# Kernel tuning notes

Measured on AMD Instinct MI355X. Metric: run time of the kernel, lower is better.

Reference implementation:

```python
import jax, jax.numpy as jnp
import numpy as np

N_C, N_A = 300000, 100000        # customers, articles
D_IN, H = 128, 128               # input feature dim, hidden dim
E, E_LBL = 2000000, 1000000      # message edges, supervision edges
BN_EPS = 1e-5


def setup_inputs() -> dict:
    key = jax.random.key(0)
    ks = jax.random.split(key, 18)
    w = lambda k, shape: jax.random.normal(k, shape, jnp.float32) * 0.05
    return {
        # node features
        "x_customer": jax.random.normal(ks[0], (N_C, D_IN), jnp.float32),
        "x_article": jax.random.normal(ks[1], (N_A, D_IN), jnp.float32),
        # customer->article edges (reverse direction reuses the same pairs)
        "edge_src_customer": jax.random.randint(ks[2], (E,), 0, N_C),
        "edge_dst_article": jax.random.randint(ks[3], (E,), 0, N_A),
        # supervision (label) edges for the decoder
        "label_customer": jax.random.randint(ks[4], (E_LBL,), 0, N_C),
        "label_article": jax.random.randint(ks[5], (E_LBL,), 0, N_A),
        # encoder layer 1 (per edge type: msg weight + self weight + bias)
        "W_msg1_ca": w(ks[6], (D_IN, H)), "W_self1_a": w(ks[7], (D_IN, H)), "b1_a": jnp.zeros((H,), jnp.float32),
        "W_msg1_ac": w(ks[8], (D_IN, H)), "W_self1_c": w(ks[9], (D_IN, H)), "b1_c": jnp.zeros((H,), jnp.float32),
        # encoder layer 2
        "W_msg2_ca": w(ks[10], (H, H)), "W_self2_a": w(ks[11], (H, H)), "b2_a": jnp.zeros((H,), jnp.float32),
        "W_msg2_ac": w(ks[12], (H, H)), "W_self2_c": w(ks[13], (H, H)), "b2_c": jnp.zeros((H,), jnp.float32),
        # per-node-type batch norm params
        "bn_gamma_c": jnp.ones((H,), jnp.float32), "bn_beta_c": jnp.zeros((H,), jnp.float32),
        "bn_gamma_a": jnp.ones((H,), jnp.float32), "bn_beta_a": jnp.zeros((H,), jnp.float32),
        # decoder MLP: Linear(2H->H) + relu, Linear(H->1)
        "W_dec1": w(ks[14], (2 * H, H)), "b_dec1": jnp.zeros((H,), jnp.float32),
        "W_dec2": w(ks[15], (H, 1)), "b_dec2": jnp.zeros((1,), jnp.float32),
    }


def _sage(x_src, x_dst, src, dst, n_dst, W_msg, W_self, b):
    # SAGEConv-style: mean-aggregate src features over incoming edges, then linear.
    agg = jax.ops.segment_sum(x_src[src], dst, num_segments=n_dst)          # [n_dst, d]
    cnt = jax.ops.segment_sum(jnp.ones((src.shape[0], 1), x_src.dtype), dst,
                              num_segments=n_dst)                            # [n_dst, 1]
    mean = agg / jnp.maximum(cnt, 1.0)
    return mean @ W_msg + x_dst @ W_self + b


def _bn(x, gamma, beta):
    # training-mode batch norm over the node axis, per channel
    mu = x.mean(axis=0)
    var = x.var(axis=0)
    return gamma * (x - mu) * jax.lax.rsqrt(var + BN_EPS) + beta


def reference(x_customer, x_article, edge_src_customer, edge_dst_article,
              label_customer, label_article,
              W_msg1_ca, W_self1_a, b1_a, W_msg1_ac, W_self1_c, b1_c,
              W_msg2_ca, W_self2_a, b2_a, W_msg2_ac, W_self2_c, b2_c,
              bn_gamma_c, bn_beta_c, bn_gamma_a, bn_beta_a,
              W_dec1, b_dec1, W_dec2, b_dec2):
    src_c, dst_a = edge_src_customer, edge_dst_article
    # hetero encoder, layer 1 (relu on all but the last layer)
    h_a = jax.nn.relu(_sage(x_customer, x_article, src_c, dst_a, N_A,
                            W_msg1_ca, W_self1_a, b1_a))
    h_c = jax.nn.relu(_sage(x_article, x_customer, dst_a, src_c, N_C,
                            W_msg1_ac, W_self1_c, b1_c))
    # layer 2 (no activation)
    z_a = _sage(h_c, h_a, src_c, dst_a, N_A, W_msg2_ca, W_self2_a, b2_a)
    z_c = _sage(h_a, h_c, dst_a, src_c, N_C, W_msg2_ac, W_self2_c, b2_c)
    # per-node-type batch norm
    z_c = _bn(z_c, bn_gamma_c, bn_beta_c)
    z_a = _bn(z_a, bn_gamma_a, bn_beta_a)
    # edge decoder: gather endpoints, concat, small MLP
    z = jnp.concatenate([z_c[label_customer], z_a[label_article]], axis=-1)  # [E_LBL, 2H]
    h = jax.nn.relu(z @ W_dec1 + b_dec1)
    return (h @ W_dec2 + b_dec2).reshape(-1)                                  # [E_LBL]
```

## Files before the change

kernel.cpp:

```cpp
#include <hip/hip_runtime.h>
#include <hip/hip_bf16.h>

#define NCN 300000
#define NAN_ 100000
#define DIM 128
#define NE 2000000
#define NL 1000000
#define NBA 1563
#define NBC 4688
#define ECH 8192
#define NCHUNK ((NE + ECH - 1) / ECH)

typedef __attribute__((ext_vector_type(8))) short bf16x8;
typedef __attribute__((ext_vector_type(4))) float f32x4;
typedef __attribute__((ext_vector_type(8))) unsigned short u16x8;
typedef __attribute__((ext_vector_type(4))) unsigned short u16x4;

static __device__ __forceinline__ unsigned short f2bf(float x){
  union { float f; unsigned u; } v; v.f = x;
  unsigned r = (v.u + 0x7FFFu + ((v.u >> 16) & 1u)) >> 16;
  return (unsigned short)r;
}
static __device__ __forceinline__ float bf2f(unsigned short h){
  union { unsigned u; float f; } v; v.u = ((unsigned)h) << 16; return v.f;
}

__global__ void k_cast(const float* __restrict__ x, unsigned short* __restrict__ y, int n4){
  int i = blockIdx.x * blockDim.x + threadIdx.x;
  if (i < n4){
    float4 v = ((const float4*)x)[i];
    u16x4 h;
    h[0] = f2bf(v.x); h[1] = f2bf(v.y); h[2] = f2bf(v.z); h[3] = f2bf(v.w);
    ((u16x4*)y)[i] = h;
  }
}

__global__ void k_bcnt(const int* __restrict__ src, const int* __restrict__ dst,
                       int* cntA, int* cntC){
  __shared__ int h[NBA + NBC];
  int t = threadIdx.x;
  for (int i = t; i < NBA + NBC; i += 256) h[i] = 0;
  __syncthreads();
  int e0 = blockIdx.x * ECH;
  int e1 = e0 + ECH < NE ? e0 + ECH : NE;
  for (int e = e0 + t; e < e1; e += 256){
    int s = src[e], d = dst[e];
    atomicAdd(&h[d >> 6], 1);
    atomicAdd(&h[NBA + (s >> 6)], 1);
  }
  __syncthreads();
  for (int i = t; i < NBA + NBC; i += 256){
    int c = h[i];
    if (c > 0){
      if (i < NBA) atomicAdd(&cntA[i], c);
      else         atomicAdd(&cntC[i - NBA], c);
    }
  }
}

__global__ void k_scan2(const int* cA, int* bA, int* uA,
                        const int* cC, int* bC, int* uC){
  const int* c; int* bs; int* cu; int n;
  if (blockIdx.x == 0){ c = cA; bs = bA; cu = uA; n = NBA; }
  else                { c = cC; bs = bC; cu = uC; n = NBC; }
  int t = threadIdx.x;
  int per = (n + 255) / 256;
  int b0 = t * per;
  int vals[19];
  int s = 0;
  for (int i = 0; i < per; i++){
    int idx = b0 + i;
    int x = (idx < n) ? c[idx] : 0;
    vals[i] = s; s += x;
  }
  int lane = t & 63, w = t >> 6;
  int inc = s;
  #pragma unroll
  for (int o = 1; o < 64; o <<= 1){ int u = __shfl_up(inc, o); if (lane >= o) inc += u; }
  __shared__ int ws[4];
  if (lane == 63) ws[w] = inc;
  __syncthreads();
  int woff = 0;
  for (int j = 0; j < w; j++) woff += ws[j];
  int ex = woff + inc - s;
  for (int i = 0; i < per; i++){
    int idx = b0 + i;
    if (idx < n){ int v = ex + vals[i]; bs[idx] = v; cu[idx] = v; }
  }
  if (t == 255) bs[n] = ex + s;
}

__global__ void k_bin(const int* __restrict__ src, const int* __restrict__ dst,
                      int* curA, int* curC, int2* binA, int2* binC){
  __shared__ int h[NBA + NBC];
  int t = threadIdx.x;
  for (int i = t; i < NBA + NBC; i += 256) h[i] = 0;
  __syncthreads();
  int e0 = blockIdx.x * ECH;
  int e1 = e0 + ECH < NE ? e0 + ECH : NE;
  for (int e = e0 + t; e < e1; e += 256){
    int s = src[e], d = dst[e];
    atomicAdd(&h[d >> 6], 1);
    atomicAdd(&h[NBA + (s >> 6)], 1);
  }
  __syncthreads();
  for (int i = t; i < NBA + NBC; i += 256){
    int c = h[i];
    if (c > 0){
      int base = (i < NBA) ? atomicAdd(&curA[i], c) : atomicAdd(&curC[i - NBA], c);
      h[i] = base;
    }
  }
  __syncthreads();
  for (int e = e0 + t; e < e1; e += 256){
    int s = src[e], d = dst[e];
    int pa = atomicAdd(&h[d >> 6], 1);
    binA[pa] = make_int2(d, s);
    int pc = atomicAdd(&h[NBA + (s >> 6)], 1);
    binC[pc] = make_int2(s, d);
  }
}

__global__ void k_csr(const int2* __restrict__ bin, const int* __restrict__ base,
                      int* __restrict__ rp, int* __restrict__ col, int ndst, int nb){
  int b = blockIdx.x;
  int d0 = b << 6;
  int beg = base[b], end = base[b + 1];
  __shared__ int deg[64], cur[64];
  int t = threadIdx.x;
  if (t < 64) deg[t] = 0;
  __syncthreads();
  for (int i = beg + t; i < end; i += 256){
    int2 p = bin[i];
    atomicAdd(&deg[p.x - d0], 1);
  }
  __syncthreads();
  if (t < 64){
    int v = deg[t];
    int inc = v;
    #pragma unroll
    for (int o = 1; o < 64; o <<= 1){ int u = __shfl_up(inc, o); if (t >= o) inc += u; }
    int ex = beg + inc - v;
    cur[t] = ex;
    if (d0 + t < ndst) rp[d0 + t] = ex;
    if (b == nb - 1 && t == 0) rp[ndst] = base[nb];
  }
  __syncthreads();
  for (int i = beg + t; i < end; i += 256){
    int2 p = bin[i];
    int pos = atomicAdd(&cur[p.x - d0], 1);
    col[pos] = p.y;
  }
}

__global__ void k_agg2(const unsigned short* __restrict__ fA, const int* __restrict__ rpA,
                       const int* __restrict__ colA, unsigned short* __restrict__ oA,
                       const unsigned short* __restrict__ fC, const int* __restrict__ rpC,
                       const int* __restrict__ colC, unsigned short* __restrict__ oC){
  int wid  = (blockIdx.x * blockDim.x + threadIdx.x) >> 6;
  int lane = threadIdx.x & 63;
  const unsigned short* feat; const int* rp; const int* col; unsigned short* outm; int d;
  if (wid < NAN_){ feat = fA; rp = rpA; col = colA; outm = oA; d = wid; }
  else if (wid < NAN_ + NCN){ feat = fC; rp = rpC; col = colC; outm = oC; d = wid - NAN_; }
  else return;
  int g  = lane >> 4;
  int cl = lane & 15;
  int beg = rp[d], end = rp[d + 1];
  float a0[8] = {0,0,0,0,0,0,0,0}, a1[8] = {0,0,0,0,0,0,0,0};
  int j = beg + g;
  for (; j + 4 < end; j += 8){
    int s0 = col[j], s1 = col[j + 4];
    u16x8 v0 = *(const u16x8*)(feat + (size_t)s0 * DIM + cl * 8);
    u16x8 v1 = *(const u16x8*)(feat + (size_t)s1 * DIM + cl * 8);
    #pragma unroll
    for (int k = 0; k < 8; k++){ a0[k] += bf2f(v0[k]); a1[k] += bf2f(v1[k]); }
  }
  if (j < end){
    int s0 = col[j];
    u16x8 v0 = *(const u16x8*)(feat + (size_t)s0 * DIM + cl * 8);
    #pragma unroll
    for (int k = 0; k < 8; k++) a0[k] += bf2f(v0[k]);
  }
  #pragma unroll
  for (int k = 0; k < 8; k++){
    float a = a0[k] + a1[k];
    a += __shfl_xor(a, 16);
    a += __shfl_xor(a, 32);
    a0[k] = a;
  }
  int dg = end - beg;
  float inv = 1.0f / (float)(dg > 1 ? dg : 1);
  if (g == 0){
    u16x8 r;
    #pragma unroll
    for (int k = 0; k < 8; k++) r[k] = f2bf(a0[k] * inv);
    *(u16x8*)(outm + (size_t)d * DIM + cl * 8) = r;
  }
}

__global__ __launch_bounds__(256) void k_gemm(
    const unsigned short* __restrict__ A, const unsigned short* __restrict__ WtA,
    const unsigned short* __restrict__ B, const unsigned short* __restrict__ WtB,
    const float* __restrict__ bias, unsigned short* out, int M, int doRelu,
    float* gsum, float* gsq)
{
  __shared__ unsigned short lA[128 * 128];
  __shared__ unsigned short lW[128 * 128];
  int t = threadIdx.x;
  int lane = t & 63, wv = t >> 6;
  int row0 = blockIdx.x * 128;
  int m = lane & 15, kq = lane >> 4;

  f32x4 acc[2][8];
  #pragma unroll
  for (int i = 0; i < 2; i++)
    #pragma unroll
    for (int j = 0; j < 8; j++) acc[i][j] = (f32x4){0.f, 0.f, 0.f, 0.f};

  const unsigned short* src = A;
  const unsigned short* wt = WtA;
  for (int pass = 0; pass < 2; ++pass){
    if (pass == 1){
      if (!B) break;
      src = B; wt = WtB;
      __syncthreads();
    }
    #pragma unroll
    for (int i = 0; i < 8; i++){
      int id = t + 256 * i;
      int r = id >> 4, c = id & 15;
      int gr = row0 + r;
      u16x8 v = {0,0,0,0,0,0,0,0};
      if (gr < M) v = *(const u16x8*)(src + (size_t)gr * DIM + c * 8);
      int pc = c ^ (r & 15);
      *(u16x8*)&lA[r * 128 + pc * 8] = v;
    }
    #pragma unroll
    for (int i = 0; i < 8; i++){
      int id = t + 256 * i;
      int n = id >> 4, cc = id & 15;
      u16x8 w = *(const u16x8*)(wt + n * 128 + cc * 8);
      int pc = cc ^ (n & 15);
      *(u16x8*)&lW[n * 128 + pc * 8] = w;
    }
    __syncthreads();
    #pragma unroll
    for (int kc = 0; kc < 4; kc++){
      int cA = kc * 4 + kq;
      int r0 = wv * 32 + m;
      int r1 = r0 + 16;
      bf16x8 a0 = *(const bf16x8*)&lA[r0 * 128 + (cA ^ m) * 8];
      bf16x8 a1 = *(const bf16x8*)&lA[r1 * 128 + (cA ^ m) * 8];
      #pragma unroll
      for (int ct = 0; ct < 8; ct++){
        int n = ct * 16 + m;
        bf16x8 bfrag = *(const bf16x8*)&lW[n * 128 + (cA ^ m) * 8];
        acc[0][ct] = __builtin_amdgcn_mfma_f32_16x16x32_bf16(a0, bfrag, acc[0][ct], 0, 0, 0);
        acc[1][ct] = __builtin_amdgcn_mfma_f32_16x16x32_bf16(a1, bfrag, acc[1][ct], 0, 0, 0);
      }
    }
  }
  float* lsum = (float*)lA;
  float* lsq  = lsum + 128;
  if (gsum){
    __syncthreads();
    if (t < 128){ lsum[t] = 0.f; lsq[t] = 0.f; }
    __syncthreads();
  }
  #pragma unroll
  for (int ct = 0; ct < 8; ct++){
    int colv = ct * 16 + m;
    float bv = bias ? bias[colv] : 0.f;
    float ps = 0.f, pq = 0.f;
    #pragma unroll
    for (int rt = 0; rt < 2; rt++){
      int rbase = row0 + wv * 32 + rt * 16 + kq * 4;
      #pragma unroll
      for (int r = 0; r < 4; r++){
        int grow = rbase + r;
        if (grow < M){
          float vo = acc[rt][ct][r] + bv;
          if (doRelu) vo = fmaxf(vo, 0.f);
          out[(size_t)grow * DIM + colv] = f2bf(vo);
          ps += vo; pq += vo * vo;
        }
      }
    }
    if (gsum){
      atomicAdd(&lsum[colv], ps);
      atomicAdd(&lsq[colv], pq);
    }
  }
  if (gsum){
    __syncthreads();
    if (t < 128){
      atomicAdd(&gsum[t], lsum[t]);
      atomicAdd(&gsq[t],  lsq[t]);
    }
  }
}

struct WtArgs { const float* s[8]; };
__global__ void k_wtrans(WtArgs a, unsigned short* dstb){
  const float* W = a.s[blockIdx.x];
  unsigned short* Wt = dstb + blockIdx.x * 16384;
  int t = threadIdx.x;
  for (int i = 0; i < 64; i++){
    int id = t + 256 * i;
    int k = id >> 7, n = id & 127;
    Wt[n * 128 + k] = f2bf(W[id]);
  }
}

__global__ void k_bnprep(const float* sums,
                         const float* gc, const float* bc,
                         const float* ga, const float* ba,
                         const float* Wd1, const float* bd1,
                         unsigned short* Wpt_c, unsigned short* Wpt_a, float* bfull){
  int n = threadIdx.x;
  __shared__ float sc[128], tc[128], sa[128], ta[128];
  {
    float mu = sums[256 + n] / (float)NCN;
    float var = sums[384 + n] / (float)NCN - mu * mu;
    float s = gc[n] * rsqrtf(var + 1e-5f);
    sc[n] = s; tc[n] = bc[n] - mu * s;
  }
  {
    float mu = sums[0 + n] / (float)NAN_;
    float var = sums[128 + n] / (float)NAN_ - mu * mu;
    float s = ga[n] * rsqrtf(var + 1e-5f);
    sa[n] = s; ta[n] = ba[n] - mu * s;
  }
  __syncthreads();
  float accv = bd1[n];
  for (int k = 0; k < 128; k++){
    float w1 = Wd1[k * DIM + n];
    float w2 = Wd1[(128 + k) * DIM + n];
    Wpt_c[n * 128 + k] = f2bf(sc[k] * w1);
    Wpt_a[n * 128 + k] = f2bf(sa[k] * w2);
    accv += tc[k] * w1 + ta[k] * w2;
  }
  bfull[n] = accv;
}

__global__ void k_dec(const int* __restrict__ lc, const int* __restrict__ la,
                      const unsigned short* __restrict__ UC, const unsigned short* __restrict__ UA,
                      const float* __restrict__ bfull, const float* __restrict__ w2,
                      const float* __restrict__ b2, float* __restrict__ out, int Etot){
  int t   = blockIdx.x * blockDim.x + threadIdx.x;
  int sl  = t & 31;
  int hw  = t >> 5;
  int nhw = (gridDim.x * blockDim.x) >> 5;
  f32x4 bb = *(const f32x4*)(bfull + sl * 4);
  f32x4 ww = *(const f32x4*)(w2 + sl * 4);
  float b2v = b2[0];
  for (int e0 = hw * 2; e0 < Etot; e0 += nhw * 2){
    int e1 = e0 + 1;
    int ic0 = lc[e0], ia0 = la[e0];
    int ic1 = lc[e1], ia1 = la[e1];
    u16x4 uc0 = *(const u16x4*)(UC + (size_t)ic0 * DIM + sl * 4);
    u16x4 ua0 = *(const u16x4*)(UA + (size_t)ia0 * DIM + sl * 4);
    u16x4 uc1 = *(const u16x4*)(UC + (size_t)ic1 * DIM + sl * 4);
    u16x4 ua1 = *(const u16x4*)(UA + (size_t)ia1 * DIM + sl * 4);
    float d0 = 0.f, d1 = 0.f;
    #pragma unroll
    for (int k = 0; k < 4; k++){
      float x0 = fmaxf(bf2f(uc0[k]) + bf2f(ua0[k]) + bb[k], 0.f);
      float x1 = fmaxf(bf2f(uc1[k]) + bf2f(ua1[k]) + bb[k], 0.f);
      d0 += x0 * ww[k];
      d1 += x1 * ww[k];
    }
    #pragma unroll
    for (int o = 16; o; o >>= 1){ d0 += __shfl_xor(d0, o); d1 += __shfl_xor(d1, o); }
    if (sl == 0){ out[e0] = d0 + b2v; out[e1] = d1 + b2v; }
  }
}

extern "C" void kernel_launch(void* const* d_in, const int* in_sizes, int n_in,
                              void* d_out, int out_size, void* d_ws, size_t ws_size,
                              hipStream_t stream){
  const float* x_c  = (const float*)d_in[0];
  const float* x_a  = (const float*)d_in[1];
  const int* e_src  = (const int*)d_in[2];
  const int* e_dst  = (const int*)d_in[3];
  const int* l_c    = (const int*)d_in[4];
  const int* l_a    = (const int*)d_in[5];
  const float* Wm1ca = (const float*)d_in[6];
  const float* Ws1a  = (const float*)d_in[7];
  const float* b1a   = (const float*)d_in[8];
  const float* Wm1ac = (const float*)d_in[9];
  const float* Ws1c  = (const float*)d_in[10];
  const float* b1c   = (const float*)d_in[11];
  const float* Wm2ca = (const float*)d_in[12];
  const float* Ws2a  = (const float*)d_in[13];
  const float* b2a   = (const float*)d_in[14];
  const float* Wm2ac = (const float*)d_in[15];
  const float* Ws2c  = (const float*)d_in[16];
  const float* b2c   = (const float*)d_in[17];
  const float* bng_c = (const float*)d_in[18];
  const float* bnb_c = (const float*)d_in[19];
  const float* bng_a = (const float*)d_in[20];
  const float* bnb_a = (const float*)d_in[21];
  const float* Wd1   = (const float*)d_in[22];
  const float* bd1   = (const float*)d_in[23];
  const float* Wd2   = (const float*)d_in[24];
  const float* bd2   = (const float*)d_in[25];
  float* out = (float*)d_out;

  char* p = (char*)d_ws;
  auto alloc = [&](size_t bytes) -> char* {
    char* r = p; p += (bytes + 255) & ~(size_t)255; return r;
  };
  int* cnt   = (int*)alloc((size_t)(NBA + NBC) * 4);
  int* cntA  = cnt;
  int* cntC  = cnt + NBA;
  int* baseA = (int*)alloc((size_t)(NBA + 1) * 4);
  int* baseC = (int*)alloc((size_t)(NBC + 1) * 4);
  int* curA  = (int*)alloc((size_t)NBA * 4);
  int* curC  = (int*)alloc((size_t)NBC * 4);
  int2* binA = (int2*)alloc((size_t)NE * 8);
  int2* binC = (int2*)alloc((size_t)NE * 8);
  int* rpa   = (int*)alloc((size_t)(NAN_ + 1) * 4);
  int* rpc   = (int*)alloc((size_t)(NCN + 1) * 4);
  int* cola  = (int*)alloc((size_t)NE * 4);
  int* colc  = (int*)alloc((size_t)NE * 4);
  unsigned short* XC = (unsigned short*)alloc((size_t)NCN * DIM * 2);
  unsigned short* XA = (unsigned short*)alloc((size_t)NAN_ * DIM * 2);
  unsigned short* MA = (unsigned short*)alloc((size_t)NAN_ * DIM * 2);
  unsigned short* MC = (unsigned short*)alloc((size_t)NCN * DIM * 2);
  unsigned short* HA = (unsigned short*)alloc((size_t)NAN_ * DIM * 2);
  unsigned short* HC = (unsigned short*)alloc((size_t)NCN * DIM * 2);
  unsigned short* Wt    = (unsigned short*)alloc(8 * 16384 * 2);
  unsigned short* Wpt_c = (unsigned short*)alloc(16384 * 2);
  unsigned short* Wpt_a = (unsigned short*)alloc(16384 * 2);
  float* bnbuf = (float*)alloc(512 * 4);
  float* bfull = (float*)alloc(128 * 4);

  k_cast<<<(NCN * DIM / 4 + 255) / 256, 256, 0, stream>>>(x_c, XC, NCN * DIM / 4);
  k_cast<<<(NAN_ * DIM / 4 + 255) / 256, 256, 0, stream>>>(x_a, XA, NAN_ * DIM / 4);

  (void)hipMemsetAsync(cnt, 0, (size_t)(NBA + NBC) * 4, stream);
  k_bcnt<<<NCHUNK, 256, 0, stream>>>(e_src, e_dst, cntA, cntC);
  k_scan2<<<2, 256, 0, stream>>>(cntA, baseA, curA, cntC, baseC, curC);
  k_bin<<<NCHUNK, 256, 0, stream>>>(e_src, e_dst, curA, curC, binA, binC);
  k_csr<<<NBA, 256, 0, stream>>>(binA, baseA, rpa, cola, NAN_, NBA);
  k_csr<<<NBC, 256, 0, stream>>>(binC, baseC, rpc, colc, NCN, NBC);

  WtArgs wa;
  wa.s[0] = Wm1ca; wa.s[1] = Ws1a; wa.s[2] = Wm1ac; wa.s[3] = Ws1c;
  wa.s[4] = Wm2ca; wa.s[5] = Ws2a; wa.s[6] = Wm2ac; wa.s[7] = Ws2c;
  k_wtrans<<<8, 256, 0, stream>>>(wa, Wt);

  int agg_blocks = ((NAN_ + NCN) * 64 + 255) / 256;
  int gba = (NAN_ + 127) / 128, gbc = (NCN + 127) / 128;

  (void)hipMemsetAsync(bnbuf, 0, 512 * 4, stream);

  k_agg2<<<agg_blocks, 256, 0, stream>>>(XC, rpa, cola, MA, XA, rpc, colc, MC);
  k_gemm<<<gba, 256, 0, stream>>>(MA, Wt + 0 * 16384, XA, Wt + 1 * 16384, b1a, HA, NAN_, 1, nullptr, nullptr);
  k_gemm<<<gbc, 256, 0, stream>>>(MC, Wt + 2 * 16384, XC, Wt + 3 * 16384, b1c, HC, NCN, 1, nullptr, nullptr);

  k_agg2<<<agg_blocks, 256, 0, stream>>>(HC, rpa, cola, MA, HA, rpc, colc, MC);
  k_gemm<<<gba, 256, 0, stream>>>(MA, Wt + 4 * 16384, HA, Wt + 5 * 16384, b2a, HA, NAN_, 0, bnbuf + 0,   bnbuf + 128);
  k_gemm<<<gbc, 256, 0, stream>>>(MC, Wt + 6 * 16384, HC, Wt + 7 * 16384, b2c, HC, NCN, 0, bnbuf + 256, bnbuf + 384);

  k_bnprep<<<1, 128, 0, stream>>>(bnbuf, bng_c, bnb_c, bng_a, bnb_a, Wd1, bd1,
                                  Wpt_c, Wpt_a, bfull);

  k_gemm<<<gba, 256, 0, stream>>>(HA, Wpt_a, nullptr, nullptr, nullptr, MA, NAN_, 0, nullptr, nullptr);
  k_gemm<<<gbc, 256, 0, stream>>>(HC, Wpt_c, nullptr, nullptr, nullptr, MC, NCN, 0, nullptr, nullptr);

  k_dec<<<4096, 256, 0, stream>>>(l_c, l_a, MC, MA, bfull, Wd2, bd2, out, NL);
}
```

Baseline: 1.380 ms.

## Fuse neighbor mean-aggregation into GEMM tile load and pack bin entries

The separate aggregation kernel is removed. Each GEMM block now gathers and averages neighbor features for its 128 rows straight into shared memory before the MFMA pass, so the intermediate aggregated matrices are never written to or read back from global memory. Bin entries are packed into 32-bit words (local destination in the high bits), which halves binning traffic. The decoder switches to 16-lane groups with 8-element loads. The risk is that the GEMM kernel now runs the irregular gather with only 4 waves per block, which may give poor latency hiding and uneven load across blocks compared with the wave-per-node aggregation kernel.

```diff
diff --git a/kernel.cpp b/kernel.cpp
--- a/kernel.cpp
+++ b/kernel.cpp
@@ -91,7 +91,7 @@
 }
 
 __global__ void k_bin(const int* __restrict__ src, const int* __restrict__ dst,
-                      int* curA, int* curC, int2* binA, int2* binC){
+                      int* curA, int* curC, unsigned* binA, unsigned* binC){
   __shared__ int h[NBA + NBC];
   int t = threadIdx.x;
   for (int i = t; i < NBA + NBC; i += 256) h[i] = 0;
@@ -115,24 +115,23 @@
   for (int e = e0 + t; e < e1; e += 256){
     int s = src[e], d = dst[e];
     int pa = atomicAdd(&h[d >> 6], 1);
-    binA[pa] = make_int2(d, s);
+    binA[pa] = ((unsigned)(d & 63) << 26) | (unsigned)s;
     int pc = atomicAdd(&h[NBA + (s >> 6)], 1);
-    binC[pc] = make_int2(s, d);
-  }
-}
-
-__global__ void k_csr(const int2* __restrict__ bin, const int* __restrict__ base,
+    binC[pc] = ((unsigned)(s & 63) << 26) | (unsigned)d;
+  }
+}
+
+__global__ void k_csr(const unsigned* __restrict__ bin, const int* __restrict__ base,
                       int* __restrict__ rp, int* __restrict__ col, int ndst, int nb){
   int b = blockIdx.x;
-  int d0 = b << 6;
   int beg = base[b], end = base[b + 1];
   __shared__ int deg[64], cur[64];
   int t = threadIdx.x;
   if (t < 64) deg[t] = 0;
   __syncthreads();
   for (int i = beg + t; i < end; i += 256){
-    int2 p = bin[i];
-    atomicAdd(&deg[p.x - d0], 1);
+    unsigned p = bin[i];
+    atomicAdd(&deg[p >> 26], 1);
   }
   __syncthreads();
   if (t < 64){
@@ -142,64 +141,23 @@
     for (int o = 1; o < 64; o <<= 1){ int u = __shfl_up(inc, o); if (t >= o) inc += u; }
     int ex = beg + inc - v;
     cur[t] = ex;
+    int d0 = b << 6;
     if (d0 + t < ndst) rp[d0 + t] = ex;
     if (b == nb - 1 && t == 0) rp[ndst] = base[nb];
   }
   __syncthreads();
   for (int i = beg + t; i < end; i += 256){
-    int2 p = bin[i];
-    int pos = atomicAdd(&cur[p.x - d0], 1);
-    col[pos] = p.y;
-  }
-}
-
-__global__ void k_agg2(const unsigned short* __restrict__ fA, const int* __restrict__ rpA,
-                       const int* __restrict__ colA, unsigned short* __restrict__ oA,
-                       const unsigned short* __restrict__ fC, const int* __restrict__ rpC,
-                       const int* __restrict__ colC, unsigned short* __restrict__ oC){
-  int wid  = (blockIdx.x * blockDim.x + threadIdx.x) >> 6;
-  int lane = threadIdx.x & 63;
-  const unsigned short* feat; const int* rp; const int* col; unsigned short* outm; int d;
-  if (wid < NAN_){ feat = fA; rp = rpA; col = colA; outm = oA; d = wid; }
-  else if (wid < NAN_ + NCN){ feat = fC; rp = rpC; col = colC; outm = oC; d = wid - NAN_; }
-  else return;
-  int g  = lane >> 4;
-  int cl = lane & 15;
-  int beg = rp[d], end = rp[d + 1];
-  float a0[8] = {0,0,0,0,0,0,0,0}, a1[8] = {0,0,0,0,0,0,0,0};
-  int j = beg + g;
-  for (; j + 4 < end; j += 8){
-    int s0 = col[j], s1 = col[j + 4];
-    u16x8 v0 = *(const u16x8*)(feat + (size_t)s0 * DIM + cl * 8);
-    u16x8 v1 = *(const u16x8*)(feat + (size_t)s1 * DIM + cl * 8);
-    #pragma unroll
-    for (int k = 0; k < 8; k++){ a0[k] += bf2f(v0[k]); a1[k] += bf2f(v1[k]); }
-  }
-  if (j < end){
-    int s0 = col[j];
-    u16x8 v0 = *(const u16x8*)(feat + (size_t)s0 * DIM + cl * 8);
-    #pragma unroll
-    for (int k = 0; k < 8; k++) a0[k] += bf2f(v0[k]);
-  }
-  #pragma unroll
-  for (int k = 0; k < 8; k++){
-    float a = a0[k] + a1[k];
-    a += __shfl_xor(a, 16);
-    a += __shfl_xor(a, 32);
-    a0[k] = a;
-  }
-  int dg = end - beg;
-  float inv = 1.0f / (float)(dg > 1 ? dg : 1);
-  if (g == 0){
-    u16x8 r;
-    #pragma unroll
-    for (int k = 0; k < 8; k++) r[k] = f2bf(a0[k] * inv);
-    *(u16x8*)(outm + (size_t)d * DIM + cl * 8) = r;
+    unsigned p = bin[i];
+    int pos = atomicAdd(&cur[p >> 26], 1);
+    col[pos] = (int)(p & 0x03FFFFFFu);
   }
 }
 
 __global__ __launch_bounds__(256) void k_gemm(
-    const unsigned short* __restrict__ A, const unsigned short* __restrict__ WtA,
+    const unsigned short* __restrict__ A,
+    const int* __restrict__ rp, const int* __restrict__ col,
+    const unsigned short* __restrict__ gfeat,
+    const unsigned short* __restrict__ WtA,
     const unsigned short* __restrict__ B, const unsigned short* __restrict__ WtB,
     const float* __restrict__ bias, unsigned short* out, int M, int doRelu,
     float* gsum, float* gsq)
@@ -217,23 +175,13 @@
     #pragma unroll
     for (int j = 0; j < 8; j++) acc[i][j] = (f32x4){0.f, 0.f, 0.f, 0.f};
 
-  const unsigned short* src = A;
-  const unsigned short* wt = WtA;
   for (int pass = 0; pass < 2; ++pass){
-    if (pass == 1){
+    const unsigned short* wt;
+    if (pass == 0) wt = WtA;
+    else {
       if (!B) break;
-      src = B; wt = WtB;
       __syncthreads();
-    }
-    #pragma unroll
-    for (int i = 0; i < 8; i++){
-      int id = t + 256 * i;
-      int r = id >> 4, c = id & 15;
-      int gr = row0 + r;
-      u16x8 v = {0,0,0,0,0,0,0,0};
-      if (gr < M) v = *(const u16x8*)(src + (size_t)gr * DIM + c * 8);
-      int pc = c ^ (r & 15);
-      *(u16x8*)&lA[r * 128 + pc * 8] = v;
+      wt = WtB;
     }
     #pragma unroll
     for (int i = 0; i < 8; i++){
@@ -242,6 +190,60 @@
       u16x8 w = *(const u16x8*)(wt + n * 128 + cc * 8);
       int pc = cc ^ (n & 15);
       *(u16x8*)&lW[n * 128 + pc * 8] = w;
+    }
+    if (pass == 1 || rp == nullptr){
+      const unsigned short* srcp = (pass == 0) ? A : B;
+      #pragma unroll
+      for (int i = 0; i < 8; i++){
+        int id = t + 256 * i;
+        int r = id >> 4, c = id & 15;
+        int gr = row0 + r;
+        u16x8 v = {0,0,0,0,0,0,0,0};
+        if (gr < M) v = *(const u16x8*)(srcp + (size_t)gr * DIM + c * 8);
+        int pc = c ^ (r & 15);
+        *(u16x8*)&lA[r * 128 + pc * 8] = v;
+      }
+    } else {
+      int g  = lane >> 4;
+      int cl = lane & 15;
+      for (int i = 0; i < 32; i++){
+        int r = wv + 4 * i;
+        int gr = row0 + r;
+        float a0[8] = {0,0,0,0,0,0,0,0}, a1[8] = {0,0,0,0,0,0,0,0};
+        int dg = 0;
+        if (gr < M){
+          int beg = rp[gr], end = rp[gr + 1];
+          dg = end - beg;
+          int j = beg + g;
+          for (; j + 4 < end; j += 8){
+            int s0 = col[j], s1 = col[j + 4];
+            u16x8 v0 = *(const u16x8*)(gfeat + (size_t)s0 * DIM + cl * 8);
+            u16x8 v1 = *(const u16x8*)(gfeat + (size_t)s1 * DIM + cl * 8);
+            #pragma unroll
+            for (int k = 0; k < 8; k++){ a0[k] += bf2f(v0[k]); a1[k] += bf2f(v1[k]); }
+          }
+          if (j < end){
+            int s0 = col[j];
+            u16x8 v0 = *(const u16x8*)(gfeat + (size_t)s0 * DIM + cl * 8);
+            #pragma unroll
+            for (int k = 0; k < 8; k++) a0[k] += bf2f(v0[k]);
+          }
+          #pragma unroll
+          for (int k = 0; k < 8; k++){
+            float a = a0[k] + a1[k];
+            a += __shfl_xor(a, 16);
+            a += __shfl_xor(a, 32);
+            a0[k] = a;
+          }
+        }
+        if (g == 0){
+          float inv = 1.0f / (float)(dg > 1 ? dg : 1);
+          u16x8 rv;
+          #pragma unroll
+          for (int k = 0; k < 8; k++) rv[k] = f2bf(a0[k] * inv);
+          *(u16x8*)&lA[r * 128 + (cl ^ (r & 15)) * 8] = rv;
+        }
+      }
     }
     __syncthreads();
     #pragma unroll
@@ -347,31 +349,32 @@
                       const unsigned short* __restrict__ UC, const unsigned short* __restrict__ UA,
                       const float* __restrict__ bfull, const float* __restrict__ w2,
                       const float* __restrict__ b2, float* __restrict__ out, int Etot){
-  int t   = blockIdx.x * blockDim.x + threadIdx.x;
-  int sl  = t & 31;
-  int hw  = t >> 5;
-  int nhw = (gridDim.x * blockDim.x) >> 5;
-  f32x4 bb = *(const f32x4*)(bfull + sl * 4);
-  f32x4 ww = *(const f32x4*)(w2 + sl * 4);
+  int t  = blockIdx.x * blockDim.x + threadIdx.x;
+  int sl = t & 15;
+  int q  = t >> 4;
+  int nq = (gridDim.x * blockDim.x) >> 4;
+  float bb[8], ww[8];
+  #pragma unroll
+  for (int k = 0; k < 8; k++){ bb[k] = bfull[sl * 8 + k]; ww[k] = w2[sl * 8 + k]; }
   float b2v = b2[0];
-  for (int e0 = hw * 2; e0 < Etot; e0 += nhw * 2){
+  for (int e0 = q * 2; e0 < Etot; e0 += nq * 2){
     int e1 = e0 + 1;
     int ic0 = lc[e0], ia0 = la[e0];
     int ic1 = lc[e1], ia1 = la[e1];
-    u16x4 uc0 = *(const u16x4*)(UC + (size_t)ic0 * DIM + sl * 4);
-    u16x4 ua0 = *(const u16x4*)(UA + (size_t)ia0 * DIM + sl * 4);
-    u16x4 uc1 = *(const u16x4*)(UC + (size_t)ic1 * DIM + sl * 4);
-    u16x4 ua1 = *(const u16x4*)(UA + (size_t)ia1 * DIM + sl * 4);
+    u16x8 uc0 = *(const u16x8*)(UC + (size_t)ic0 * DIM + sl * 8);
+    u16x8 ua0 = *(const u16x8*)(UA + (size_t)ia0 * DIM + sl * 8);
+    u16x8 uc1 = *(const u16x8*)(UC + (size_t)ic1 * DIM + sl * 8);
+    u16x8 ua1 = *(const u16x8*)(UA + (size_t)ia1 * DIM + sl * 8);
     float d0 = 0.f, d1 = 0.f;
     #pragma unroll
-    for (int k = 0; k < 4; k++){
+    for (int k = 0; k < 8; k++){
       float x0 = fmaxf(bf2f(uc0[k]) + bf2f(ua0[k]) + bb[k], 0.f);
       float x1 = fmaxf(bf2f(uc1[k]) + bf2f(ua1[k]) + bb[k], 0.f);
       d0 += x0 * ww[k];
       d1 += x1 * ww[k];
     }
     #pragma unroll
-    for (int o = 16; o; o >>= 1){ d0 += __shfl_xor(d0, o); d1 += __shfl_xor(d1, o); }
+    for (int o = 8; o; o >>= 1){ d0 += __shfl_xor(d0, o); d1 += __shfl_xor(d1, o); }
     if (sl == 0){ out[e0] = d0 + b2v; out[e1] = d1 + b2v; }
   }
 }
@@ -418,23 +421,25 @@
   int* baseC = (int*)alloc((size_t)(NBC + 1) * 4);
   int* curA  = (int*)alloc((size_t)NBA * 4);
   int* curC  = (int*)alloc((size_t)NBC * 4);
-  int2* binA = (int2*)alloc((size_t)NE * 8);
-  int2* binC = (int2*)alloc((size_t)NE * 8);
+  unsigned* binA = (unsigned*)alloc((size_t)NE * 4);
+  unsigned* binC = (unsigned*)alloc((size_t)NE * 4);
   int* rpa   = (int*)alloc((size_t)(NAN_ + 1) * 4);
   int* rpc   = (int*)alloc((size_t)(NCN + 1) * 4);
   int* cola  = (int*)alloc((size_t)NE * 4);
   int* colc  = (int*)alloc((size_t)NE * 4);
   unsigned short* XC = (unsigned short*)alloc((size_t)NCN * DIM * 2);
   unsigned short* XA = (unsigned short*)alloc((size_t)NAN_ * DIM * 2);
-  unsigned short* MA = (unsigned short*)alloc((size_t)NAN_ * DIM * 2);
-  unsigned short* MC = (unsigned short*)alloc((size_t)NCN * DIM * 2);
   unsigned short* HA = (unsigned short*)alloc((size_t)NAN_ * DIM * 2);
   unsigned short* HC = (unsigned short*)alloc((size_t)NCN * DIM * 2);
+  unsigned short* UA = (unsigned short*)alloc((size_t)NAN_ * DIM * 2);
+  unsigned short* UC = (unsigned short*)alloc((size_t)NCN * DIM * 2);
   unsigned short* Wt    = (unsigned short*)alloc(8 * 16384 * 2);
   unsigned short* Wpt_c = (unsigned short*)alloc(16384 * 2);
   unsigned short* Wpt_a = (unsigned short*)alloc(16384 * 2);
   float* bnbuf = (float*)alloc(512 * 4);
   float* bfull = (float*)alloc(128 * 4);
+  unsigned short* ZA = XA;
+  unsigned short* ZC = XC;
 
   k_cast<<<(NCN * DIM / 4 + 255) / 256, 256, 0, stream>>>(x_c, XC, NCN * DIM / 4);
   k_cast<<<(NAN_ * DIM / 4 + 255) / 256, 256, 0, stream>>>(x_a, XA, NAN_ * DIM / 4);
@@ -451,24 +456,26 @@
   wa.s[4] = Wm2ca; wa.s[5] = Ws2a; wa.s[6] = Wm2ac; wa.s[7] = Ws2c;
   k_wtrans<<<8, 256, 0, stream>>>(wa, Wt);
 
-  int agg_blocks = ((NAN_ + NCN) * 64 + 255) / 256;
   int gba = (NAN_ + 127) / 128, gbc = (NCN + 127) / 128;
-
   (void)hipMemsetAsync(bnbuf, 0, 512 * 4, stream);
 
-  k_agg2<<<agg_blocks, 256, 0, stream>>>(XC, rpa, cola, MA, XA, rpc, colc, MC);
-  k_gemm<<<gba, 256, 0, stream>>>(MA, Wt + 0 * 16384, XA, Wt + 1 * 16384, b1a, HA, NAN_, 1, nullptr, nullptr);
-  k_gemm<<<gbc, 256, 0, stream>>>(MC, Wt + 2 * 16384, XC, Wt + 3 * 16384, b1c, HC, NCN, 1, nullptr, nullptr);
-
-  k_agg2<<<agg_blocks, 256, 0, stream>>>(HC, rpa, cola, MA, HA, rpc, colc, MC);
-  k_gemm<<<gba, 256, 0, stream>>>(MA, Wt + 4 * 16384, HA, Wt + 5 * 16384, b2a, HA, NAN_, 0, bnbuf + 0,   bnbuf + 128);
-  k_gemm<<<gbc, 256, 0, stream>>>(MC, Wt + 6 * 16384, HC, Wt + 7 * 16384, b2c, HC, NCN, 0, bnbuf + 256, bnbuf + 384);
+  k_gemm<<<gba, 256, 0, stream>>>(nullptr, rpa, cola, XC, Wt + 0 * 16384,
+                                  XA, Wt + 1 * 16384, b1a, HA, NAN_, 1, nullptr, nullptr);
+  k_gemm<<<gbc, 256, 0, stream>>>(nullptr, rpc, colc, XA, Wt + 2 * 16384,
+                                  XC, Wt + 3 * 16384, b1c, HC, NCN, 1, nullptr, nullptr);
+
+  k_gemm<<<gba, 256, 0, stream>>>(nullptr, rpa, cola, HC, Wt + 4 * 16384,
+                                  HA, Wt + 5 * 16384, b2a, ZA, NAN_, 0, bnbuf + 0,   bnbuf + 128);
+  k_gemm<<<gbc, 256, 0, stream>>>(nullptr, rpc, colc, HA, Wt + 6 * 16384,
+                                  HC, Wt + 7 * 16384, b2c, ZC, NCN, 0, bnbuf + 256, bnbuf + 384);
 
   k_bnprep<<<1, 128, 0, stream>>>(bnbuf, bng_c, bnb_c, bng_a, bnb_a, Wd1, bd1,
                                   Wpt_c, Wpt_a, bfull);
 
-  k_gemm<<<gba, 256, 0, stream>>>(HA, Wpt_a, nullptr, nullptr, nullptr, MA, NAN_, 0, nullptr, nullptr);
-  k_gemm<<<gbc, 256, 0, stream>>>(HC, Wpt_c, nullptr, nullptr, nullptr, MC, NCN, 0, nullptr, nullptr);
-
-  k_dec<<<4096, 256, 0, stream>>>(l_c, l_a, MC, MA, bfull, Wd2, bd2, out, NL);
-}
+  k_gemm<<<gba, 256, 0, stream>>>(ZA, nullptr, nullptr, nullptr, Wpt_a,
+                                  nullptr, nullptr, nullptr, UA, NAN_, 0, nullptr, nullptr);
+  k_gemm<<<gbc, 256, 0, stream>>>(ZC, nullptr, nullptr, nullptr, Wpt_c,
+                                  nullptr, nullptr, nullptr, UC, NCN, 0, nullptr, nullptr);
+
+  k_dec<<<4096, 256, 0, stream>>>(l_c, l_a, UC, UA, bfull, Wd2, bd2, out, NL);
+}
```

Result: slower. 1.867 ms (+35.2%).
